# Kernel tuning notes

Hardware: AMD Instinct MI355X
Metric: run time of the kernel (lower is better)

The kernel has to match this reference:

```python
import jax, jax.numpy as jnp
import numpy as np

N0 = N1 = 100000
D = H = 512
E = 1000000
NEG_SLOPE = 0.01  # nn.LeakyReLU default

def _lin(k, fin, fout):
    kw, kb = jax.random.split(k)
    s = 1.0 / np.sqrt(fin)
    W = jax.random.uniform(kw, (fin, fout), jnp.float32, -s, s)
    b = jax.random.uniform(kb, (fout,), jnp.float32, -s, s)
    return W, b

def setup_inputs() -> dict:
    key = jax.random.key(0)
    ks = jax.random.split(key, 18)
    inp = {
        "x_n0": jax.random.normal(ks[0], (N0, D), jnp.float32),
        "x_n1": jax.random.normal(ks[1], (N1, D), jnp.float32),
        "ei_01": jnp.stack([jax.random.randint(ks[2], (E,), 0, N0),
                            jax.random.randint(ks[3], (E,), 0, N1)]),
        "ei_10": jnp.stack([jax.random.randint(ks[4], (E,), 0, N1),
                            jax.random.randint(ks[5], (E,), 0, N0)]),
    }
    i = 6
    for layer, din in (("l1", D), ("l2", H)):
        for mt in ("01", "10"):
            Wn, bn = _lin(ks[i], din, H); i += 1
            Ws, bs = _lin(ks[i], din, H); i += 1
            Wu, bu = _lin(ks[i], 2 * H, H); i += 1
            inp[f"{layer}_{mt}_Wn"] = Wn; inp[f"{layer}_{mt}_bn"] = bn
            inp[f"{layer}_{mt}_Ws"] = Ws; inp[f"{layer}_{mt}_bs"] = bs
            inp[f"{layer}_{mt}_Wu"] = Wu; inp[f"{layer}_{mt}_bu"] = bu
    return inp

def _sage(x_src, x_dst, ei, Wn, bn, Ws, bs, Wu, bu):
    # HeteroSAGEConv: gather src feats along edges, mean-aggregate onto dst,
    # then lin_neigh(agg) || lin_self(x_dst) -> lin_update
    n_dst = x_dst.shape[0]
    agg = jax.ops.segment_sum(x_src[ei[0]], ei[1], num_segments=n_dst)  # [n_dst, d]
    cnt = jax.ops.segment_sum(jnp.ones((ei.shape[1],), x_src.dtype), ei[1], num_segments=n_dst)
    agg = agg / jnp.maximum(cnt, 1.0)[:, None]
    h = jnp.concatenate([agg @ Wn + bn, x_dst @ Ws + bs], axis=-1)  # [n_dst, 2H]
    return h @ Wu + bu

def _lrelu(x):
    return jax.nn.leaky_relu(x, NEG_SLOPE)

def reference(x_n0, x_n1, ei_01, ei_10,
              l1_01_Wn, l1_01_bn, l1_01_Ws, l1_01_bs, l1_01_Wu, l1_01_bu,
              l1_10_Wn, l1_10_bn, l1_10_Ws, l1_10_bs, l1_10_Wu, l1_10_bu,
              l2_01_Wn, l2_01_bn, l2_01_Ws, l2_01_bs, l2_01_Wu, l2_01_bu,
              l2_10_Wn, l2_10_bn, l2_10_Ws, l2_10_bs, l2_10_Wu, l2_10_bu):
    # dropout is identity in eval mode (p handled outside the math)
    h0, h1 = _lrelu(x_n0), _lrelu(x_n1)
    o1 = _sage(h0, h1, ei_01, l1_01_Wn, l1_01_bn, l1_01_Ws, l1_01_bs, l1_01_Wu, l1_01_bu)
    o0 = _sage(h1, h0, ei_10, l1_10_Wn, l1_10_bn, l1_10_Ws, l1_10_bs, l1_10_Wu, l1_10_bu)
    h0, h1 = _lrelu(o0), _lrelu(o1)
    o1 = _sage(h0, h1, ei_01, l2_01_Wn, l2_01_bn, l2_01_Ws, l2_01_bs, l2_01_Wu, l2_01_bu)
    o0 = _sage(h1, h0, ei_10, l2_10_Wn, l2_10_bn, l2_10_Ws, l2_10_bs, l2_10_Wu, l2_10_bu)
    return (o0, o1)
```

## Files before the change

kernel.cpp:

```cpp
#include <hip/hip_runtime.h>


typedef unsigned short ushort_t;
using short8 = __attribute__((ext_vector_type(8))) short;
using f32x4  = __attribute__((ext_vector_type(4))) float;

typedef __attribute__((address_space(3))) void lds_void;
typedef __attribute__((address_space(1))) void gbl_void;

__device__ __forceinline__ void gload16(const void* g, void* l) {
  __builtin_amdgcn_global_load_lds((gbl_void*)g, (lds_void*)l, 16, 0, 0);
}

__device__ __forceinline__ float bf2f(unsigned short u) {
  union { unsigned i; float f; } c; c.i = ((unsigned)u) << 16; return c.f;
}
__device__ __forceinline__ unsigned short f2bf(float f) {
  union { float f; unsigned i; } c; c.f = f;
  unsigned r = c.i + 0x7FFF + ((c.i >> 16) & 1);
  return (unsigned short)(r >> 16);
}
__device__ __forceinline__ unsigned pack2(float a, float b) {
  return (unsigned)f2bf(a) | ((unsigned)f2bf(b) << 16);
}

template <int MODE>
__device__ __forceinline__ void gemm_core(
    const ushort_t* __restrict__ A0, const ushort_t* __restrict__ A1,
    int lda, int ka0,
    const ushort_t* __restrict__ BT, int ldb,
    const float* __restrict__ bias,
    void* __restrict__ outp, int ldo, int Mreal, int Ktiles,
    int bm, int bn)
{
  __shared__ __align__(16) ushort_t lA[2][128 * 32];
  __shared__ __align__(16) ushort_t lB[2][128 * 32];
  const int tid = threadIdx.x;
  const int w = tid >> 6;
  const int l = tid & 63;
  const int srow = (l >> 2);
  const int scol = (l & 3) * 8;
  const int m_base = bm * 128;
  const int n_base = bn * 128;

  f32x4 acc[4][4] = {};

  auto stage = [&](int buf, int kt) {
    const int k0 = kt * 32;
    const ushort_t* As; int kk;
    if (k0 < ka0) { As = A0; kk = k0; } else { As = A1; kk = k0 - ka0; }
#pragma unroll
    for (int r = 0; r < 2; ++r) {
      const int row = r * 64 + w * 16 + srow;
      gload16(As + (size_t)(m_base + row) * lda + (kk + scol),
              &lA[buf][(r * 64 + w * 16) * 32]);
      gload16(BT + (size_t)(n_base + row) * ldb + (k0 + scol),
              &lB[buf][(r * 64 + w * 16) * 32]);
    }
  };

  const int wm0 = (w & 1) * 64;
  const int wn0 = (w >> 1) * 64;
  const int fr  = l & 15;
  const int fko = (l >> 4) * 8;

  auto compute = [&](int buf) {
    short8 a[4], b[4];
#pragma unroll
    for (int t = 0; t < 4; ++t) {
      a[t] = *(const short8*)&lA[buf][(wm0 + t * 16 + fr) * 32 + fko];
      b[t] = *(const short8*)&lB[buf][(wn0 + t * 16 + fr) * 32 + fko];
    }
#pragma unroll
    for (int mt = 0; mt < 4; ++mt)
#pragma unroll
      for (int nt = 0; nt < 4; ++nt)
        acc[mt][nt] = __builtin_amdgcn_mfma_f32_16x16x32_bf16(
            a[mt], b[nt], acc[mt][nt], 0, 0, 0);
  };

  stage(0, 0);
  __syncthreads();

  for (int kt = 0; kt < Ktiles; kt += 2) {
    stage(1, kt + 1);
    compute(0);
    __syncthreads();
    if (kt + 2 < Ktiles) stage(0, kt + 2);
    compute(1);
    __syncthreads();
  }

  const int quad = l >> 4;
  const int c15 = l & 15;
#pragma unroll
  for (int nt = 0; nt < 4; ++nt) {
    const int gn = n_base + wn0 + nt * 16 + c15;
    const float bv = (MODE == 2) ? 0.0f : bias[gn];
#pragma unroll
    for (int mt = 0; mt < 4; ++mt) {
#pragma unroll
      for (int r = 0; r < 4; ++r) {
        const int gm = m_base + wm0 + mt * 16 + quad * 4 + r;
        float v = acc[mt][nt][r] + bv;
        if (MODE == 0) {
          if (gm < Mreal) ((float*)outp)[(size_t)gm * ldo + gn] = v;
        } else if (MODE == 1) {
          float t = v > 0.0f ? v : 0.01f * v;
          ((ushort_t*)outp)[(size_t)gm * ldo + gn] = f2bf(t);
        } else {
          ((ushort_t*)outp)[(size_t)gn * ldo + gm] = f2bf(v);
        }
      }
    }
  }
}

struct GemmArgs {
  const ushort_t* A0; const ushort_t* A1; int lda; int ka0;
  const ushort_t* BT; int ldb; const float* bias;
  void* out; int ldo; int Mreal; int Ktiles;
};

template <int MODE>
__global__ __launch_bounds__(256) void gemm_kernel(GemmArgs g) {
  const int nwg = gridDim.x;
  const int orig = blockIdx.x;
  const int q = nwg >> 3, r = nwg & 7, x = orig & 7;
  const int swz = (x < r ? x * (q + 1) : r * (q + 1) + (x - r) * q) + (orig >> 3);
  const int bn = swz & 3;
  const int bm = swz >> 2;
  gemm_core<MODE>(g.A0, g.A1, g.lda, g.ka0, g.BT, g.ldb, g.bias,
                  g.out, g.ldo, g.Mreal, g.Ktiles, bm, bn);
}

__global__ __launch_bounds__(256) void fold_gemm_kernel(
    const ushort_t* __restrict__ WnWs, const ushort_t* __restrict__ WuT,
    ushort_t* __restrict__ WfT)
{
  const int z = blockIdx.z, sage = z >> 1, half = z & 1;
  gemm_core<2>(WnWs + (size_t)sage * 524288 + half * 262144, nullptr, 512, (1 << 30),
               WuT + (size_t)sage * 524288 + half * 512, 1024, nullptr,
               WfT + (size_t)sage * 524288 + half * 512, 1024, 512, 16,
               blockIdx.x, blockIdx.y);
}

__global__ void lrelu_cast_kernel(const float* __restrict__ x,
                                  ushort_t* __restrict__ h, int n4)
{
  const int i = blockIdx.x * 256 + threadIdx.x;
  if (i >= n4) return;
  const float4 v = ((const float4*)x)[i];
  float a = v.x > 0.f ? v.x : 0.01f * v.x;
  float b = v.y > 0.f ? v.y : 0.01f * v.y;
  float c = v.z > 0.f ? v.z : 0.01f * v.z;
  float d = v.w > 0.f ? v.w : 0.01f * v.w;
  uint2 o; o.x = pack2(a, b); o.y = pack2(c, d);
  ((uint2*)h)[i] = o;
}

struct EdgeArgs {
  const int* src0; const int* dst0;
  const int* src1; const int* dst1;
  int* cnt0; int* cnt1;
  int* indptr0; int* indptr1;
  int* fill0; int* fill1;
  int* esrc0; int* esrc1;
  int E; int nd0; int nd1;
};

__global__ void hist_kernel(EdgeArgs ea) {
  const int dir = blockIdx.y;
  const int e = blockIdx.x * 256 + threadIdx.x;
  if (e >= ea.E) return;
  const int* dst = dir ? ea.dst1 : ea.dst0;
  int* cnt = dir ? ea.cnt1 : ea.cnt0;
  atomicAdd(&cnt[dst[e]], 1);
}

__global__ __launch_bounds__(1024) void scan_kernel(EdgeArgs ea) {
  const int dir = blockIdx.y;
  const int* cnt = dir ? ea.cnt1 : ea.cnt0;
  int* indptr = dir ? ea.indptr1 : ea.indptr0;
  int* fill = dir ? ea.fill1 : ea.fill0;
  const int n = dir ? ea.nd1 : ea.nd0;
  __shared__ int sd[1024];
  const int t = threadIdx.x;
  const int chunk = (n + 1023) >> 10;
  const int start = t * chunk;
  const int end = (start + chunk < n) ? (start + chunk) : n;
  int sum = 0;
  for (int i = start; i < end; ++i) sum += cnt[i];
  sd[t] = sum;
  __syncthreads();
  for (int off = 1; off < 1024; off <<= 1) {
    int v = (t >= off) ? sd[t - off] : 0;
    __syncthreads();
    sd[t] += v;
    __syncthreads();
  }
  int run = sd[t] - sum;
  for (int i = start; i < end; ++i) { indptr[i] = run; fill[i] = run; run += cnt[i]; }
  if (t == 0) indptr[n] = ea.E;
}

__global__ void scatter_kernel(EdgeArgs ea) {
  const int dir = blockIdx.y;
  const int e = blockIdx.x * 256 + threadIdx.x;
  if (e >= ea.E) return;
  const int* dst = dir ? ea.dst1 : ea.dst0;
  const int* src = dir ? ea.src1 : ea.src0;
  int* fill = dir ? ea.fill1 : ea.fill0;
  int* esrc = dir ? ea.esrc1 : ea.esrc0;
  const int pos = atomicAdd(&fill[dst[e]], 1);
  esrc[pos] = src[e];
}

__device__ __forceinline__ void acc8(float* a, uint4 u) {
  a[0] += bf2f((unsigned short)(u.x & 0xffff)); a[1] += bf2f((unsigned short)(u.x >> 16));
  a[2] += bf2f((unsigned short)(u.y & 0xffff)); a[3] += bf2f((unsigned short)(u.y >> 16));
  a[4] += bf2f((unsigned short)(u.z & 0xffff)); a[5] += bf2f((unsigned short)(u.z >> 16));
  a[6] += bf2f((unsigned short)(u.w & 0xffff)); a[7] += bf2f((unsigned short)(u.w >> 16));
}

__global__ __launch_bounds__(256) void agg_kernel(
    const ushort_t* __restrict__ hsrc, const int* __restrict__ indptr,
    const int* __restrict__ esrc, ushort_t* __restrict__ out, int ndst)
{
  const int widx = blockIdx.x * 4 + (threadIdx.x >> 6);
  const int l = threadIdx.x & 63;
  if (widx >= ndst) return;
  const int s = indptr[widx], e = indptr[widx + 1];
  float a[8] = {0.f, 0.f, 0.f, 0.f, 0.f, 0.f, 0.f, 0.f};
  int i = s;
  for (; i + 1 < e; i += 2) {
    const int r0 = esrc[i], r1 = esrc[i + 1];
    const uint4 u0 = *(const uint4*)(hsrc + (size_t)r0 * 512 + l * 8);
    const uint4 u1 = *(const uint4*)(hsrc + (size_t)r1 * 512 + l * 8);
    acc8(a, u0); acc8(a, u1);
  }
  if (i < e) {
    const uint4 u = *(const uint4*)(hsrc + (size_t)esrc[i] * 512 + l * 8);
    acc8(a, u);
  }
  const int deg = e - s;
  const float sc = 1.0f / (float)(deg > 1 ? deg : 1);
  uint4 o;
  o.x = pack2(a[0] * sc, a[1] * sc); o.y = pack2(a[2] * sc, a[3] * sc);
  o.z = pack2(a[4] * sc, a[5] * sc); o.w = pack2(a[6] * sc, a[7] * sc);
  *(uint4*)(out + (size_t)widx * 512 + l * 8) = o;
}

struct CastArgs { const float* Wn[4]; const float* Ws[4]; const float* Wu[4]; };

__global__ void cast_all_kernel(CastArgs ca, ushort_t* __restrict__ WnWs,
                                ushort_t* __restrict__ WuT)
{
  const int sage = blockIdx.z;
  const int type = blockIdx.y;
  const int idx = blockIdx.x * 256 + threadIdx.x;
  if (type < 2) {
    if (idx >= 512 * 512) return;
    const float* src = type == 0 ? ca.Wn[sage] : ca.Ws[sage];
    WnWs[(size_t)sage * 524288 + type * 262144 + idx] = f2bf(src[idx]);
  } else {
    if (idx >= 1024 * 512) return;
    const int k = idx >> 9, n = idx & 511;
    WuT[(size_t)sage * 524288 + (size_t)n * 1024 + k] = f2bf(ca.Wu[sage][idx]);
  }
}

struct BiasArgs { const float* bn[4]; const float* bs[4];
                  const float* Wu[4]; const float* bu[4]; };

__global__ void bias_fold_kernel(BiasArgs ba, float* __restrict__ cf) {
  const int sage = blockIdx.y;
  const int n = blockIdx.x * 256 + threadIdx.x;
  const float* Wu = ba.Wu[sage];
  const float* bn = ba.bn[sage];
  const float* bs = ba.bs[sage];
  float s = ba.bu[sage][n];
  for (int j = 0; j < 512; ++j)
    s += bn[j] * Wu[(size_t)j * 512 + n] + bs[j] * Wu[(size_t)(512 + j) * 512 + n];
  cf[sage * 512 + n] = s;
}

extern "C" void kernel_launch(void* const* d_in, const int* in_sizes, int n_in,
                              void* d_out, int out_size, void* d_ws, size_t ws_size,
                              hipStream_t stream)
{
  const int Dm = 512;
  const int N0 = in_sizes[0] / Dm;
  const int N1 = in_sizes[1] / Dm;
  const int E  = in_sizes[2] / 2;
  const int NMAX = N0 > N1 ? N0 : N1;
  const int MP = ((NMAX + 127) / 128) * 128;
  const int Mtiles = MP / 128;

  auto al = [](size_t x) { return (x + 255) & ~(size_t)255; };
  const size_t BIG = (size_t)MP * 512 * sizeof(ushort_t);

  char* p = (char*)d_ws;
  ushort_t* h0 = (ushort_t*)p; p += BIG;
  ushort_t* h1 = (ushort_t*)p; p += BIG;
  ushort_t* bA = (ushort_t*)p; p += BIG;
  ushort_t* bB = (ushort_t*)p; p += BIG;
  ushort_t* bC = (ushort_t*)p; p += BIG;
  ushort_t* WnWs = (ushort_t*)p; p += al((size_t)4 * 524288 * 2);
  ushort_t* WuT  = (ushort_t*)p; p += al((size_t)4 * 524288 * 2);
  ushort_t* WfT  = (ushort_t*)p; p += al((size_t)4 * 524288 * 2);
  float* cf = (float*)p; p += al(4 * 512 * sizeof(float));
  char* cnt_base = p;
  int* cnt0 = (int*)p; p += al((size_t)N1 * 4);
  int* cnt1 = (int*)p; p += al((size_t)N0 * 4);
  const size_t cnt_bytes = (size_t)(p - cnt_base);
  int* ip0 = (int*)p; p += al((size_t)(N1 + 1) * 4);
  int* ip1 = (int*)p; p += al((size_t)(N0 + 1) * 4);
  int* fl0 = (int*)p; p += al((size_t)N1 * 4);
  int* fl1 = (int*)p; p += al((size_t)N0 * 4);
  int* es0 = (int*)p; p += al((size_t)E * 4);
  int* es1 = (int*)p; p += al((size_t)E * 4);
  if ((size_t)(p - (char*)d_ws) > ws_size) return;

  const float* x0 = (const float*)d_in[0];
  const float* x1 = (const float*)d_in[1];
  const int* ei01 = (const int*)d_in[2];
  const int* ei10 = (const int*)d_in[3];

  CastArgs ca; BiasArgs ba;
  for (int s = 0; s < 4; ++s) {
    const int base = 4 + 6 * s;
    ca.Wn[s] = (const float*)d_in[base + 0];
    ba.bn[s] = (const float*)d_in[base + 1];
    ca.Ws[s] = (const float*)d_in[base + 2];
    ba.bs[s] = (const float*)d_in[base + 3];
    ca.Wu[s] = (const float*)d_in[base + 4];
    ba.Wu[s] = ca.Wu[s];
    ba.bu[s] = (const float*)d_in[base + 5];
  }

  EdgeArgs ea;
  ea.src0 = ei01; ea.dst0 = ei01 + E;
  ea.src1 = ei10; ea.dst1 = ei10 + E;
  ea.cnt0 = cnt0; ea.cnt1 = cnt1;
  ea.indptr0 = ip0; ea.indptr1 = ip1;
  ea.fill0 = fl0; ea.fill1 = fl1;
  ea.esrc0 = es0; ea.esrc1 = es1;
  ea.E = E; ea.nd0 = N1; ea.nd1 = N0;

  hipMemsetAsync(cnt_base, 0, cnt_bytes, stream);
  lrelu_cast_kernel<<<dim3((N0 * Dm / 4 + 255) / 256), 256, 0, stream>>>(x0, h0, N0 * Dm / 4);
  lrelu_cast_kernel<<<dim3((N1 * Dm / 4 + 255) / 256), 256, 0, stream>>>(x1, h1, N1 * Dm / 4);
  hist_kernel<<<dim3((E + 255) / 256, 2), 256, 0, stream>>>(ea);
  scan_kernel<<<dim3(1, 2), 1024, 0, stream>>>(ea);
  scatter_kernel<<<dim3((E + 255) / 256, 2), 256, 0, stream>>>(ea);

  cast_all_kernel<<<dim3(2048, 3, 4), 256, 0, stream>>>(ca, WnWs, WuT);
  fold_gemm_kernel<<<dim3(4, 4, 8), 256, 0, stream>>>(WnWs, WuT, WfT);
  bias_fold_kernel<<<dim3(2, 4), 256, 0, stream>>>(ba, cf);

  agg_kernel<<<dim3((N1 + 3) / 4), 256, 0, stream>>>(h0, ip0, es0, bA, N1);
  agg_kernel<<<dim3((N0 + 3) / 4), 256, 0, stream>>>(h1, ip1, es1, bB, N0);

  GemmArgs g;
  g.lda = 512; g.ka0 = 512; g.ldb = 1024; g.Ktiles = 32; g.ldo = 512;
  const int NWG = Mtiles * 4;
  g.A0 = bA; g.A1 = h1; g.BT = WfT + 0 * 524288; g.bias = cf + 0;
  g.out = bC; g.Mreal = N1;
  gemm_kernel<1><<<dim3(NWG), 256, 0, stream>>>(g);
  g.A0 = bB; g.A1 = h0; g.BT = WfT + 1 * 524288; g.bias = cf + 512;
  g.out = bA; g.Mreal = N0;
  gemm_kernel<1><<<dim3(NWG), 256, 0, stream>>>(g);

  agg_kernel<<<dim3((N1 + 3) / 4), 256, 0, stream>>>(bA, ip0, es0, h0, N1);
  agg_kernel<<<dim3((N0 + 3) / 4), 256, 0, stream>>>(bC, ip1, es1, h1, N0);

  g.A0 = h0; g.A1 = bC; g.BT = WfT + 2 * 524288; g.bias = cf + 1024;
  g.out = (float*)d_out + (size_t)N0 * 512; g.Mreal = N1;
  gemm_kernel<0><<<dim3(NWG), 256, 0, stream>>>(g);
  g.A0 = h1; g.A1 = bA; g.BT = WfT + 3 * 524288; g.bias = cf + 1536;
  g.out = (float*)d_out; g.Mreal = N0;
  gemm_kernel<0><<<dim3(NWG), 256, 0, stream>>>(g);
}
```

Measured before the change: 2.647 ms.

## Use 8-wave GEMM workgroups with 64x32 wave tiles and unroll aggregation by four

The MFMA GEMM workgroup grows from 256 to 512 threads, so eight waves now share the same 128x128 tile. Each wave computes a 64x32 sub-tile, and staging becomes one 16-byte load per thread. Launch bounds request four resident blocks per CU to raise occupancy and hide latency. The trade-off is less register-level reuse per wave, more LDS fragment reads per MFMA, and tighter register limits. The neighbour-aggregation gather loop is also unrolled to four independent row loads per iteration to raise memory-level parallelism.

```diff
diff --git a/kernel.cpp b/kernel.cpp
--- a/kernel.cpp
+++ b/kernel.cpp
@@ -38,43 +38,40 @@
   const int tid = threadIdx.x;
   const int w = tid >> 6;
   const int l = tid & 63;
-  const int srow = (l >> 2);
-  const int scol = (l & 3) * 8;
+  const int srow = tid >> 2;
+  const int scol = (tid & 3) * 8;
   const int m_base = bm * 128;
   const int n_base = bn * 128;
 
-  f32x4 acc[4][4] = {};
+  f32x4 acc[4][2] = {};
 
   auto stage = [&](int buf, int kt) {
     const int k0 = kt * 32;
     const ushort_t* As; int kk;
     if (k0 < ka0) { As = A0; kk = k0; } else { As = A1; kk = k0 - ka0; }
-#pragma unroll
-    for (int r = 0; r < 2; ++r) {
-      const int row = r * 64 + w * 16 + srow;
-      gload16(As + (size_t)(m_base + row) * lda + (kk + scol),
-              &lA[buf][(r * 64 + w * 16) * 32]);
-      gload16(BT + (size_t)(n_base + row) * ldb + (k0 + scol),
-              &lB[buf][(r * 64 + w * 16) * 32]);
-    }
+    gload16(As + (size_t)(m_base + srow) * lda + (kk + scol),
+            &lA[buf][srow * 32 + scol]);
+    gload16(BT + (size_t)(n_base + srow) * ldb + (k0 + scol),
+            &lB[buf][srow * 32 + scol]);
   };
 
   const int wm0 = (w & 1) * 64;
-  const int wn0 = (w >> 1) * 64;
+  const int wn0 = (w >> 1) * 32;
   const int fr  = l & 15;
   const int fko = (l >> 4) * 8;
 
   auto compute = [&](int buf) {
-    short8 a[4], b[4];
-#pragma unroll
-    for (int t = 0; t < 4; ++t) {
+    short8 a[4], b[2];
+#pragma unroll
+    for (int t = 0; t < 4; ++t)
       a[t] = *(const short8*)&lA[buf][(wm0 + t * 16 + fr) * 32 + fko];
+#pragma unroll
+    for (int t = 0; t < 2; ++t)
       b[t] = *(const short8*)&lB[buf][(wn0 + t * 16 + fr) * 32 + fko];
-    }
 #pragma unroll
     for (int mt = 0; mt < 4; ++mt)
 #pragma unroll
-      for (int nt = 0; nt < 4; ++nt)
+      for (int nt = 0; nt < 2; ++nt)
         acc[mt][nt] = __builtin_amdgcn_mfma_f32_16x16x32_bf16(
             a[mt], b[nt], acc[mt][nt], 0, 0, 0);
   };
@@ -94,7 +91,7 @@
   const int quad = l >> 4;
   const int c15 = l & 15;
 #pragma unroll
-  for (int nt = 0; nt < 4; ++nt) {
+  for (int nt = 0; nt < 2; ++nt) {
     const int gn = n_base + wn0 + nt * 16 + c15;
     const float bv = (MODE == 2) ? 0.0f : bias[gn];
 #pragma unroll
@@ -123,7 +120,7 @@
 };
 
 template <int MODE>
-__global__ __launch_bounds__(256) void gemm_kernel(GemmArgs g) {
+__global__ __launch_bounds__(512, 4) void gemm_kernel(GemmArgs g) {
   const int nwg = gridDim.x;
   const int orig = blockIdx.x;
   const int q = nwg >> 3, r = nwg & 7, x = orig & 7;
@@ -134,7 +131,7 @@
                   g.out, g.ldo, g.Mreal, g.Ktiles, bm, bn);
 }
 
-__global__ __launch_bounds__(256) void fold_gemm_kernel(
+__global__ __launch_bounds__(512, 4) void fold_gemm_kernel(
     const ushort_t* __restrict__ WnWs, const ushort_t* __restrict__ WuT,
     ushort_t* __restrict__ WfT)
 {
@@ -233,13 +230,15 @@
   const int s = indptr[widx], e = indptr[widx + 1];
   float a[8] = {0.f, 0.f, 0.f, 0.f, 0.f, 0.f, 0.f, 0.f};
   int i = s;
-  for (; i + 1 < e; i += 2) {
-    const int r0 = esrc[i], r1 = esrc[i + 1];
+  for (; i + 3 < e; i += 4) {
+    const int r0 = esrc[i], r1 = esrc[i + 1], r2 = esrc[i + 2], r3 = esrc[i + 3];
     const uint4 u0 = *(const uint4*)(hsrc + (size_t)r0 * 512 + l * 8);
     const uint4 u1 = *(const uint4*)(hsrc + (size_t)r1 * 512 + l * 8);
-    acc8(a, u0); acc8(a, u1);
-  }
-  if (i < e) {
+    const uint4 u2 = *(const uint4*)(hsrc + (size_t)r2 * 512 + l * 8);
+    const uint4 u3 = *(const uint4*)(hsrc + (size_t)r3 * 512 + l * 8);
+    acc8(a, u0); acc8(a, u1); acc8(a, u2); acc8(a, u3);
+  }
+  for (; i < e; ++i) {
     const uint4 u = *(const uint4*)(hsrc + (size_t)esrc[i] * 512 + l * 8);
     acc8(a, u);
   }
@@ -356,7 +355,7 @@
   scatter_kernel<<<dim3((E + 255) / 256, 2), 256, 0, stream>>>(ea);
 
   cast_all_kernel<<<dim3(2048, 3, 4), 256, 0, stream>>>(ca, WnWs, WuT);
-  fold_gemm_kernel<<<dim3(4, 4, 8), 256, 0, stream>>>(WnWs, WuT, WfT);
+  fold_gemm_kernel<<<dim3(4, 4, 8), 512, 0, stream>>>(WnWs, WuT, WfT);
   bias_fold_kernel<<<dim3(2, 4), 256, 0, stream>>>(ba, cf);
 
   agg_kernel<<<dim3((N1 + 3) / 4), 256, 0, stream>>>(h0, ip0, es0, bA, N1);
@@ -367,18 +366,18 @@
   const int NWG = Mtiles * 4;
   g.A0 = bA; g.A1 = h1; g.BT = WfT + 0 * 524288; g.bias = cf + 0;
   g.out = bC; g.Mreal = N1;
-  gemm_kernel<1><<<dim3(NWG), 256, 0, stream>>>(g);
+  gemm_kernel<1><<<dim3(NWG), 512, 0, stream>>>(g);
   g.A0 = bB; g.A1 = h0; g.BT = WfT + 1 * 524288; g.bias = cf + 512;
   g.out = bA; g.Mreal = N0;
-  gemm_kernel<1><<<dim3(NWG), 256, 0, stream>>>(g);
+  gemm_kernel<1><<<dim3(NWG), 512, 0, stream>>>(g);
 
   agg_kernel<<<dim3((N1 + 3) / 4), 256, 0, stream>>>(bA, ip0, es0, h0, N1);
   agg_kernel<<<dim3((N0 + 3) / 4), 256, 0, stream>>>(bC, ip1, es1, h1, N0);
 
   g.A0 = h0; g.A1 = bC; g.BT = WfT + 2 * 524288; g.bias = cf + 1024;
   g.out = (float*)d_out + (size_t)N0 * 512; g.Mreal = N1;
-  gemm_kernel<0><<<dim3(NWG), 256, 0, stream>>>(g);
+  gemm_kernel<0><<<dim3(NWG), 512, 0, stream>>>(g);
   g.A0 = h1; g.A1 = bA; g.BT = WfT + 3 * 524288; g.bias = cf + 1536;
   g.out = (float*)d_out; g.Mreal = N0;
-  gemm_kernel<0><<<dim3(NWG), 256, 0, stream>>>(g);
-}
+  gemm_kernel<0><<<dim3(NWG), 512, 0, stream>>>(g);
+}
```

Measured after the change: 2.510 ms. -5.2%, faster.
